# Optimization experiments

Hardware: AMD Instinct MI355X
Metric: run time of the kernel (lower is better)

## Reference

```python
import jax, jax.numpy as jnp
import numpy as np

NUM_CHANS = 64
LAG = 5
HIDDEN = [32, 32]  # module appends a final 1-channel layer
BATCH = 16
T = 2048


def setup_inputs() -> dict:
    key = jax.random.key(0)
    ks = jax.random.split(key, 7)
    p, h0, h1 = NUM_CHANS, HIDDEN[0], HIDDEN[1]
    # Per-network weights stacked along leading axis n = num_series = p.
    # Xavier-ish scale for layer 0 (Conv1d(p, h0, lag)), default-ish for rest.
    s0 = float(np.sqrt(2.0 / (p * LAG + h0)))
    return {
        "X": jax.random.normal(ks[0], (BATCH, T, p), dtype=jnp.float32),
        "W0": jax.random.normal(ks[1], (p, h0, p, LAG), dtype=jnp.float32) * s0,
        "b0": jax.random.normal(ks[2], (p, h0), dtype=jnp.float32) * 0.01,
        "W1": jax.random.normal(ks[3], (p, h1, h0), dtype=jnp.float32) * float(np.sqrt(1.0 / h0)),
        "b1": jax.random.normal(ks[4], (p, h1), dtype=jnp.float32) * 0.01,
        "W2": jax.random.normal(ks[5], (p, 1, h1), dtype=jnp.float32) * float(np.sqrt(1.0 / h1)),
        "b2": jax.random.normal(ks[6], (p, 1), dtype=jnp.float32) * 0.01,
    }


def reference(X, W0, b0, W1, b1, W2, b2):
    # X: [B, T, p]. Each of n=p networks: Conv1d(p,h0,lag) -> ReLU -> Conv1d(h0,h1,1)
    # -> ReLU -> Conv1d(h1,1,1); outputs concatenated along last dim.
    lag = W0.shape[-1]
    Tout = X.shape[1] - lag + 1  # valid conv output length
    # Sliding windows: Xwin[b,t,c,l] = X[b, t+l, c]  -> [B, Tout, p, lag]
    Xwin = jnp.stack([X[:, l:l + Tout, :] for l in range(lag)], axis=-1)
    # Layer 0 across all n networks at once: [B, n, Tout, h0]
    h = jnp.einsum('btcl,nhcl->bnth', Xwin, W0) + b0[None, :, None, :]
    # 1x1 conv layers (per-network dense along channel dim)
    h = jax.nn.relu(h)
    h = jnp.einsum('bnti,noi->bnto', h, W1) + b1[None, :, None, :]
    h = jax.nn.relu(h)
    h = jnp.einsum('bnti,noi->bnto', h, W2) + b2[None, :, None, :]  # [B, n, Tout, 1]
    # concat along dim 2 of (batch, Tout, 1) per network -> (B, Tout, n)
    return jnp.transpose(h[..., 0], (0, 2, 1))
```

## Files before the change

### kernel.cpp

```cpp
#include <hip/hip_runtime.h>

#define NCH 64
#define LAG 5
#define H0 32
#define H1 32
#define TIN 2048
#define TOUT 2044
#define NBATCH 16

#define XSTRIDE 72

typedef __attribute__((ext_vector_type(8))) short short8;
typedef __attribute__((ext_vector_type(4))) short short4v;
typedef __attribute__((ext_vector_type(4))) float f32x4;

__device__ __forceinline__ unsigned short f2bf(float f) {
    unsigned u = __float_as_uint(f);
    u += 0x7fffu + ((u >> 16) & 1u);
    return (unsigned short)(u >> 16);
}

__device__ __forceinline__ unsigned pack2bf_relu(float a, float b) {
    unsigned ua = __float_as_uint(fmaxf(a, 0.0f)) + 0x8000u;
    unsigned ub = __float_as_uint(fmaxf(b, 0.0f)) + 0x8000u;
    return __builtin_amdgcn_perm(ub, ua, 0x07060302u);
}

__device__ __forceinline__ short4v pack4bf_relu(const f32x4& v) {
    union { short4v s; unsigned u[2]; } cv;
    cv.u[0] = pack2bf_relu(v[0], v[1]);
    cv.u[1] = pack2bf_relu(v[2], v[3]);
    return cv.s;
}

__global__ __launch_bounds__(256) void prep_all(
    const float* __restrict__ X,  unsigned short* __restrict__ Xpad,
    const float* __restrict__ W0, unsigned short* __restrict__ W0b,
    const float* __restrict__ W1, unsigned short* __restrict__ W1b,
    const float* __restrict__ W2, unsigned short* __restrict__ W2b)
{
    const int bx = blockIdx.x;
    if (bx < 2048) {
        int j = bx * 256 + threadIdx.x;
        int row = j >> 4, seg = j & 15;
        float4 x = *(const float4*)(X + (size_t)j * 4);
        unsigned long long v = (unsigned long long)f2bf(x.x)
                             | ((unsigned long long)f2bf(x.y) << 16)
                             | ((unsigned long long)f2bf(x.z) << 32)
                             | ((unsigned long long)f2bf(x.w) << 48);
        *(unsigned long long*)(Xpad + (size_t)row * XSTRIDE + seg * 4) = v;
    } else if (bx < 2560) {
        int j = (bx - 2048) * 256 + threadIdx.x;
        int nh = j >> 6, c = j & 63;
        const float* src = W0 + (size_t)j * LAG;
        unsigned short* dst = W0b + nh * 320 + c;
        #pragma unroll
        for (int l = 0; l < LAG; ++l) dst[l * 64] = f2bf(src[l]);
    } else if (bx < 2592) {
        int i = ((bx - 2560) * 256 + threadIdx.x) * 8;
        float4 a = *(const float4*)(W1 + i);
        float4 b = *(const float4*)(W1 + i + 4);
        unsigned long long v0 = (unsigned long long)f2bf(a.x)
                              | ((unsigned long long)f2bf(a.y) << 16)
                              | ((unsigned long long)f2bf(a.z) << 32)
                              | ((unsigned long long)f2bf(a.w) << 48);
        unsigned long long v1 = (unsigned long long)f2bf(b.x)
                              | ((unsigned long long)f2bf(b.y) << 16)
                              | ((unsigned long long)f2bf(b.z) << 32)
                              | ((unsigned long long)f2bf(b.w) << 48);
        *(unsigned long long*)(W1b + i)     = v0;
        *(unsigned long long*)(W1b + i + 4) = v1;
    } else {
        int i = threadIdx.x * 8;
        float4 a = *(const float4*)(W2 + i);
        float4 b = *(const float4*)(W2 + i + 4);
        unsigned long long v0 = (unsigned long long)f2bf(a.x)
                              | ((unsigned long long)f2bf(a.y) << 16)
                              | ((unsigned long long)f2bf(a.z) << 32)
                              | ((unsigned long long)f2bf(a.w) << 48);
        unsigned long long v1 = (unsigned long long)f2bf(b.x)
                              | ((unsigned long long)f2bf(b.y) << 16)
                              | ((unsigned long long)f2bf(b.z) << 32)
                              | ((unsigned long long)f2bf(b.w) << 48);
        *(unsigned long long*)(W2b + i)     = v0;
        *(unsigned long long*)(W2b + i + 4) = v1;
    }
}

__global__ __launch_bounds__(256, 3) void mlp_mfma(
    const unsigned short* __restrict__ Xpad,
    const unsigned short* __restrict__ W0b,
    const unsigned short* __restrict__ W1b,
    const unsigned short* __restrict__ W2b,
    const float* __restrict__ b0, const float* __restrict__ b1,
    const float* __restrict__ b2, float* __restrict__ out)
{
    __shared__ __align__(16) unsigned short xs[37 * 512];
    __shared__ __align__(8)  unsigned short yt[256][4];

    const int tileid = blockIdx.x;
    const int ng     = blockIdx.y;
    const int b      = tileid >> 3;
    const int t0     = (tileid & 7) * 256;
    const int tid    = threadIdx.x;
    const int wave   = tid >> 6;
    const int lane   = tid & 63;
    const int quad   = lane >> 4;
    const int l15    = lane & 15;

    {
        const char* srcb = (const char*)(Xpad + (size_t)(b * TIN + t0) * XSTRIDE);
        #pragma unroll 1
        for (int i = wave; i < 37; i += 4) {
            __builtin_amdgcn_global_load_lds(
                (const __attribute__((address_space(1))) unsigned int*)(srcb + i * 1024 + lane * 16),
                (__attribute__((address_space(3))) unsigned int*)((char*)xs + i * 1024),
                16, 0, 0);
        }
    }

    const int n = ng * 4 + wave;
    short8 B0[10][2];
    const unsigned short* wp0 = W0b + (n * H0 + l15) * (NCH * LAG) + quad * 8;
    #pragma unroll
    for (int ks = 0; ks < 10; ++ks) {
        B0[ks][0] = *(const short8*)(wp0 + ks * 32);
        B0[ks][1] = *(const short8*)(wp0 + 16 * (NCH * LAG) + ks * 32);
    }
    short4v A1[2][2];
    #pragma unroll
    for (int of = 0; of < 2; ++of)
        #pragma unroll
        for (int kf = 0; kf < 2; ++kf)
            A1[of][kf] = *(const short4v*)(W1b + (n * H1 + of * 16 + l15) * H0 + kf * 16 + quad * 4);
    short4v A2[2];
    #pragma unroll
    for (int kf = 0; kf < 2; ++kf)
        A2[kf] = *(const short4v*)(W2b + n * H1 + kf * 16 + quad * 4);
    f32x4 b0q[2], b1q[2];
    #pragma unroll
    for (int nf = 0; nf < 2; ++nf) b0q[nf] = *(const f32x4*)(b0 + (size_t)n * H0 + nf * 16 + quad * 4);
    #pragma unroll
    for (int of = 0; of < 2; ++of) b1q[of] = *(const f32x4*)(b1 + (size_t)n * H1 + of * 16 + quad * 4);
    const float b2s = b2[n];

    __syncthreads();

    const int vmax = (t0 == 1792) ? 251 : 255;

    #pragma unroll 1
    for (int chunk = 0; chunk < 8; ++chunk) {
        int rowoff[2];
        #pragma unroll
        for (int mf = 0; mf < 2; ++mf) {
            int i = chunk * 32 + mf * 16 + l15;
            i = i < vmax ? i : vmax;
            rowoff[mf] = i * XSTRIDE + quad * 8;
        }

        f32x4 acc[2][2];
        #pragma unroll
        for (int mf = 0; mf < 2; ++mf) {
            acc[mf][0] = b0q[0];
            acc[mf][1] = b0q[1];
        }
        __builtin_amdgcn_s_setprio(1);
        #pragma unroll
        for (int ks = 0; ks < 10; ++ks) {
            const int xoff = (ks >> 1) * XSTRIDE + (ks & 1) * 32;
            #pragma unroll
            for (int mf = 0; mf < 2; ++mf) {
                short8 Xf = *(const short8*)&xs[rowoff[mf] + xoff];
                acc[mf][0] = __builtin_amdgcn_mfma_f32_16x16x32_bf16(B0[ks][0], Xf, acc[mf][0], 0, 0, 0);
                acc[mf][1] = __builtin_amdgcn_mfma_f32_16x16x32_bf16(B0[ks][1], Xf, acc[mf][1], 0, 0, 0);
            }
        }
        __builtin_amdgcn_s_setprio(0);

        #pragma unroll
        for (int mf = 0; mf < 2; ++mf) {
            short4v Bh0 = pack4bf_relu(acc[mf][0]);
            short4v Bh1 = pack4bf_relu(acc[mf][1]);

            f32x4 D1[2] = { b1q[0], b1q[1] };
            __builtin_amdgcn_s_setprio(1);
            D1[0] = __builtin_amdgcn_mfma_f32_16x16x16bf16_1k(A1[0][0], Bh0, D1[0], 0, 0, 0);
            D1[0] = __builtin_amdgcn_mfma_f32_16x16x16bf16_1k(A1[0][1], Bh1, D1[0], 0, 0, 0);
            D1[1] = __builtin_amdgcn_mfma_f32_16x16x16bf16_1k(A1[1][0], Bh0, D1[1], 0, 0, 0);
            D1[1] = __builtin_amdgcn_mfma_f32_16x16x16bf16_1k(A1[1][1], Bh1, D1[1], 0, 0, 0);
            __builtin_amdgcn_s_setprio(0);

            short4v Bg0 = pack4bf_relu(D1[0]);
            short4v Bg1 = pack4bf_relu(D1[1]);

            f32x4 D2 = (f32x4){ b2s, b2s, b2s, b2s };
            __builtin_amdgcn_s_setprio(1);
            D2 = __builtin_amdgcn_mfma_f32_16x16x16bf16_1k(A2[0], Bg0, D2, 0, 0, 0);
            D2 = __builtin_amdgcn_mfma_f32_16x16x16bf16_1k(A2[1], Bg1, D2, 0, 0, 0);
            __builtin_amdgcn_s_setprio(0);

            if (quad == 0)
                yt[chunk * 32 + mf * 16 + l15][wave] = f2bf(D2[0]);
        }
    }
    __syncthreads();

    int t = t0 + tid;
    if (t < TOUT) {
        ushort4 v = *(const ushort4*)yt[tid];
        float4 o;
        o.x = __uint_as_float((unsigned)v.x << 16);
        o.y = __uint_as_float((unsigned)v.y << 16);
        o.z = __uint_as_float((unsigned)v.z << 16);
        o.w = __uint_as_float((unsigned)v.w << 16);
        *(float4*)&out[((size_t)(b * TOUT + t)) * NCH + ng * 4] = o;
    }
}

extern "C" void kernel_launch(void* const* d_in, const int* in_sizes, int n_in,
                              void* d_out, int out_size, void* d_ws, size_t ws_size,
                              hipStream_t stream)
{
    const float* X  = (const float*)d_in[0];
    const float* W0 = (const float*)d_in[1];
    const float* b0 = (const float*)d_in[2];
    const float* W1 = (const float*)d_in[3];
    const float* b1 = (const float*)d_in[4];
    const float* W2 = (const float*)d_in[5];
    const float* b2 = (const float*)d_in[6];
    float* out = (float*)d_out;

    unsigned short* Xpad = (unsigned short*)d_ws;
    unsigned short* W0b  = (unsigned short*)((char*)d_ws + 4726784);
    unsigned short* W1b  = (unsigned short*)((char*)d_ws + 6037504);
    unsigned short* W2b  = (unsigned short*)((char*)d_ws + 6168576);

    prep_all<<<2593, 256, 0, stream>>>(X, Xpad, W0, W0b, W1, W1b, W2, W2b);
    mlp_mfma<<<dim3(128, 16), 256, 0, stream>>>(Xpad, W0b, W1b, W2b, b0, b1, b2, out);
}
```

Measured before the change: 118.0 us.

## Process two networks per wave to reuse staged X tiles across networks

Each wave now handles two networks instead of one, so every block covers eight output channels and the grid's network dimension halves. Each X fragment read from LDS feeds four MFMAs instead of two, and the global-to-LDS staging of X is done half as often overall. The cost is twice the weight registers per wave (W0 fragments double), so the occupancy hint drops from 3 to 2 blocks per CU and the grid has half as many blocks. The output writes become two float4 stores per thread.

```diff
diff --git a/kernel.cpp b/kernel.cpp
--- a/kernel.cpp
+++ b/kernel.cpp
@@ -87,7 +87,7 @@
     }
 }
 
-__global__ __launch_bounds__(256, 3) void mlp_mfma(
+__global__ __launch_bounds__(256, 2) void mlp_mfma(
     const unsigned short* __restrict__ Xpad,
     const unsigned short* __restrict__ W0b,
     const unsigned short* __restrict__ W1b,
@@ -96,7 +96,7 @@
     const float* __restrict__ b2, float* __restrict__ out)
 {
     __shared__ __align__(16) unsigned short xs[37 * 512];
-    __shared__ __align__(8)  unsigned short yt[256][4];
+    __shared__ __align__(16) unsigned short yt[256][8];
 
     const int tileid = blockIdx.x;
     const int ng     = blockIdx.y;
@@ -119,30 +119,34 @@
         }
     }
 
-    const int n = ng * 4 + wave;
-    short8 B0[10][2];
-    const unsigned short* wp0 = W0b + (n * H0 + l15) * (NCH * LAG) + quad * 8;
+    short8 B0[2][10][2];
+    short4v A1[2][2][2];
+    short4v A2[2][2];
+    f32x4 b0q[2][2], b1q[2][2];
+    float b2s[2];
     #pragma unroll
-    for (int ks = 0; ks < 10; ++ks) {
-        B0[ks][0] = *(const short8*)(wp0 + ks * 32);
-        B0[ks][1] = *(const short8*)(wp0 + 16 * (NCH * LAG) + ks * 32);
-    }
-    short4v A1[2][2];
-    #pragma unroll
-    for (int of = 0; of < 2; ++of)
+    for (int net = 0; net < 2; ++net) {
+        const int n = ng * 8 + net * 4 + wave;
+        const unsigned short* wp0 = W0b + (n * H0 + l15) * (NCH * LAG) + quad * 8;
+        #pragma unroll
+        for (int ks = 0; ks < 10; ++ks) {
+            B0[net][ks][0] = *(const short8*)(wp0 + ks * 32);
+            B0[net][ks][1] = *(const short8*)(wp0 + 16 * (NCH * LAG) + ks * 32);
+        }
+        #pragma unroll
+        for (int of = 0; of < 2; ++of)
+            #pragma unroll
+            for (int kf = 0; kf < 2; ++kf)
+                A1[net][of][kf] = *(const short4v*)(W1b + (n * H1 + of * 16 + l15) * H0 + kf * 16 + quad * 4);
         #pragma unroll
         for (int kf = 0; kf < 2; ++kf)
-            A1[of][kf] = *(const short4v*)(W1b + (n * H1 + of * 16 + l15) * H0 + kf * 16 + quad * 4);
-    short4v A2[2];
-    #pragma unroll
-    for (int kf = 0; kf < 2; ++kf)
-        A2[kf] = *(const short4v*)(W2b + n * H1 + kf * 16 + quad * 4);
-    f32x4 b0q[2], b1q[2];
-    #pragma unroll
-    for (int nf = 0; nf < 2; ++nf) b0q[nf] = *(const f32x4*)(b0 + (size_t)n * H0 + nf * 16 + quad * 4);
-    #pragma unroll
-    for (int of = 0; of < 2; ++of) b1q[of] = *(const f32x4*)(b1 + (size_t)n * H1 + of * 16 + quad * 4);
-    const float b2s = b2[n];
+            A2[net][kf] = *(const short4v*)(W2b + n * H1 + kf * 16 + quad * 4);
+        #pragma unroll
+        for (int nf = 0; nf < 2; ++nf) b0q[net][nf] = *(const f32x4*)(b0 + (size_t)n * H0 + nf * 16 + quad * 4);
+        #pragma unroll
+        for (int of = 0; of < 2; ++of) b1q[net][of] = *(const f32x4*)(b1 + (size_t)n * H1 + of * 16 + quad * 4);
+        b2s[net] = b2[n];
+    }
 
     __syncthreads();
 
@@ -150,70 +154,70 @@
 
     #pragma unroll 1
     for (int chunk = 0; chunk < 8; ++chunk) {
-        int rowoff[2];
         #pragma unroll
         for (int mf = 0; mf < 2; ++mf) {
-            int i = chunk * 32 + mf * 16 + l15;
-            i = i < vmax ? i : vmax;
-            rowoff[mf] = i * XSTRIDE + quad * 8;
-        }
-
-        f32x4 acc[2][2];
-        #pragma unroll
-        for (int mf = 0; mf < 2; ++mf) {
-            acc[mf][0] = b0q[0];
-            acc[mf][1] = b0q[1];
-        }
-        __builtin_amdgcn_s_setprio(1);
-        #pragma unroll
-        for (int ks = 0; ks < 10; ++ks) {
-            const int xoff = (ks >> 1) * XSTRIDE + (ks & 1) * 32;
-            #pragma unroll
-            for (int mf = 0; mf < 2; ++mf) {
-                short8 Xf = *(const short8*)&xs[rowoff[mf] + xoff];
-                acc[mf][0] = __builtin_amdgcn_mfma_f32_16x16x32_bf16(B0[ks][0], Xf, acc[mf][0], 0, 0, 0);
-                acc[mf][1] = __builtin_amdgcn_mfma_f32_16x16x32_bf16(B0[ks][1], Xf, acc[mf][1], 0, 0, 0);
+            const int irow = chunk * 32 + mf * 16 + l15;
+            const int ic   = irow < vmax ? irow : vmax;
+            const int rowoff = ic * XSTRIDE + quad * 8;
+
+            f32x4 acc[2][2];
+            #pragma unroll
+            for (int net = 0; net < 2; ++net) {
+                acc[net][0] = b0q[net][0];
+                acc[net][1] = b0q[net][1];
+            }
+            __builtin_amdgcn_s_setprio(1);
+            #pragma unroll
+            for (int ks = 0; ks < 10; ++ks) {
+                const int xoff = (ks >> 1) * XSTRIDE + (ks & 1) * 32;
+                short8 Xf = *(const short8*)&xs[rowoff + xoff];
+                acc[0][0] = __builtin_amdgcn_mfma_f32_16x16x32_bf16(B0[0][ks][0], Xf, acc[0][0], 0, 0, 0);
+                acc[0][1] = __builtin_amdgcn_mfma_f32_16x16x32_bf16(B0[0][ks][1], Xf, acc[0][1], 0, 0, 0);
+                acc[1][0] = __builtin_amdgcn_mfma_f32_16x16x32_bf16(B0[1][ks][0], Xf, acc[1][0], 0, 0, 0);
+                acc[1][1] = __builtin_amdgcn_mfma_f32_16x16x32_bf16(B0[1][ks][1], Xf, acc[1][1], 0, 0, 0);
+            }
+            __builtin_amdgcn_s_setprio(0);
+
+            #pragma unroll
+            for (int net = 0; net < 2; ++net) {
+                short4v Bh0 = pack4bf_relu(acc[net][0]);
+                short4v Bh1 = pack4bf_relu(acc[net][1]);
+
+                f32x4 D1[2] = { b1q[net][0], b1q[net][1] };
+                D1[0] = __builtin_amdgcn_mfma_f32_16x16x16bf16_1k(A1[net][0][0], Bh0, D1[0], 0, 0, 0);
+                D1[0] = __builtin_amdgcn_mfma_f32_16x16x16bf16_1k(A1[net][0][1], Bh1, D1[0], 0, 0, 0);
+                D1[1] = __builtin_amdgcn_mfma_f32_16x16x16bf16_1k(A1[net][1][0], Bh0, D1[1], 0, 0, 0);
+                D1[1] = __builtin_amdgcn_mfma_f32_16x16x16bf16_1k(A1[net][1][1], Bh1, D1[1], 0, 0, 0);
+
+                short4v Bg0 = pack4bf_relu(D1[0]);
+                short4v Bg1 = pack4bf_relu(D1[1]);
+
+                f32x4 D2 = (f32x4){ b2s[net], b2s[net], b2s[net], b2s[net] };
+                D2 = __builtin_amdgcn_mfma_f32_16x16x16bf16_1k(A2[net][0], Bg0, D2, 0, 0, 0);
+                D2 = __builtin_amdgcn_mfma_f32_16x16x16bf16_1k(A2[net][1], Bg1, D2, 0, 0, 0);
+
+                if (quad == 0)
+                    yt[irow][wave + net * 4] = f2bf(D2[0]);
             }
         }
-        __builtin_amdgcn_s_setprio(0);
-
-        #pragma unroll
-        for (int mf = 0; mf < 2; ++mf) {
-            short4v Bh0 = pack4bf_relu(acc[mf][0]);
-            short4v Bh1 = pack4bf_relu(acc[mf][1]);
-
-            f32x4 D1[2] = { b1q[0], b1q[1] };
-            __builtin_amdgcn_s_setprio(1);
-            D1[0] = __builtin_amdgcn_mfma_f32_16x16x16bf16_1k(A1[0][0], Bh0, D1[0], 0, 0, 0);
-            D1[0] = __builtin_amdgcn_mfma_f32_16x16x16bf16_1k(A1[0][1], Bh1, D1[0], 0, 0, 0);
-            D1[1] = __builtin_amdgcn_mfma_f32_16x16x16bf16_1k(A1[1][0], Bh0, D1[1], 0, 0, 0);
-            D1[1] = __builtin_amdgcn_mfma_f32_16x16x16bf16_1k(A1[1][1], Bh1, D1[1], 0, 0, 0);
-            __builtin_amdgcn_s_setprio(0);
-
-            short4v Bg0 = pack4bf_relu(D1[0]);
-            short4v Bg1 = pack4bf_relu(D1[1]);
-
-            f32x4 D2 = (f32x4){ b2s, b2s, b2s, b2s };
-            __builtin_amdgcn_s_setprio(1);
-            D2 = __builtin_amdgcn_mfma_f32_16x16x16bf16_1k(A2[0], Bg0, D2, 0, 0, 0);
-            D2 = __builtin_amdgcn_mfma_f32_16x16x16bf16_1k(A2[1], Bg1, D2, 0, 0, 0);
-            __builtin_amdgcn_s_setprio(0);
-
-            if (quad == 0)
-                yt[chunk * 32 + mf * 16 + l15][wave] = f2bf(D2[0]);
-        }
     }
     __syncthreads();
 
     int t = t0 + tid;
     if (t < TOUT) {
-        ushort4 v = *(const ushort4*)yt[tid];
-        float4 o;
-        o.x = __uint_as_float((unsigned)v.x << 16);
-        o.y = __uint_as_float((unsigned)v.y << 16);
-        o.z = __uint_as_float((unsigned)v.z << 16);
-        o.w = __uint_as_float((unsigned)v.w << 16);
-        *(float4*)&out[((size_t)(b * TOUT + t)) * NCH + ng * 4] = o;
+        short8 v = *(const short8*)yt[tid];
+        float4 o0, o1;
+        o0.x = __uint_as_float((unsigned)(unsigned short)v[0] << 16);
+        o0.y = __uint_as_float((unsigned)(unsigned short)v[1] << 16);
+        o0.z = __uint_as_float((unsigned)(unsigned short)v[2] << 16);
+        o0.w = __uint_as_float((unsigned)(unsigned short)v[3] << 16);
+        o1.x = __uint_as_float((unsigned)(unsigned short)v[4] << 16);
+        o1.y = __uint_as_float((unsigned)(unsigned short)v[5] << 16);
+        o1.z = __uint_as_float((unsigned)(unsigned short)v[6] << 16);
+        o1.w = __uint_as_float((unsigned)(unsigned short)v[7] << 16);
+        size_t base = ((size_t)(b * TOUT + t)) * NCH + ng * 8;
+        *(float4*)&out[base]     = o0;
+        *(float4*)&out[base + 4] = o1;
     }
 }
 
@@ -236,5 +240,5 @@
     unsigned short* W2b  = (unsigned short*)((char*)d_ws + 6168576);
 
     prep_all<<<2593, 256, 0, stream>>>(X, Xpad, W0, W0b, W1, W1b, W2, W2b);
-    mlp_mfma<<<dim3(128, 16), 256, 0, stream>>>(Xpad, W0b, W1b, W2b, b0, b1, b2, out);
-}
+    mlp_mfma<<<dim3(128, 8), 256, 0, stream>>>(Xpad, W0b, W1b, W2b, b0, b1, b2, out);
+}
```

Result: slower. 124.8 us (+5.8%).

## Software-pipeline layer-0 MFMA with tail layers using double-buffered accumulators

Applied to the files above, without the earlier changes.

Restructures the chunk loop into a two-stage software pipeline: the layer-0 MFMA accumulation for the next chunk is issued before the layer-1/2 tail of the current chunk, using two accumulator sets. This lets independent MFMA work hide the dependency chain of the small tail matmuls. It also removes the setprio hints, drops the quad==0 guard by widening the yt scratch to 8 columns (quads 1-3 write to otherwise-unused columns 4-7), and lowers launch_bounds occupancy from 3 to 2 to give room for the extra registers. Lower occupancy may reduce latency hiding across waves.

```diff
diff --git a/kernel.cpp b/kernel.cpp
--- a/kernel.cpp
+++ b/kernel.cpp
@@ -87,7 +87,7 @@
     }
 }
 
-__global__ __launch_bounds__(256, 3) void mlp_mfma(
+__global__ __launch_bounds__(256, 2) void mlp_mfma(
     const unsigned short* __restrict__ Xpad,
     const unsigned short* __restrict__ W0b,
     const unsigned short* __restrict__ W1b,
@@ -96,7 +96,7 @@
     const float* __restrict__ b2, float* __restrict__ out)
 {
     __shared__ __align__(16) unsigned short xs[37 * 512];
-    __shared__ __align__(8)  unsigned short yt[256][4];
+    __shared__ __align__(16) unsigned short yt[256][8];
 
     const int tileid = blockIdx.x;
     const int ng     = blockIdx.y;
@@ -107,6 +107,7 @@
     const int lane   = tid & 63;
     const int quad   = lane >> 4;
     const int l15    = lane & 15;
+    const int colw   = wave + (quad ? 4 : 0);
 
     {
         const char* srcb = (const char*)(Xpad + (size_t)(b * TIN + t0) * XSTRIDE);
@@ -148,61 +149,58 @@
 
     const int vmax = (t0 == 1792) ? 251 : 255;
 
-    #pragma unroll 1
-    for (int chunk = 0; chunk < 8; ++chunk) {
-        int rowoff[2];
-        #pragma unroll
-        for (int mf = 0; mf < 2; ++mf) {
-            int i = chunk * 32 + mf * 16 + l15;
-            i = i < vmax ? i : vmax;
-            rowoff[mf] = i * XSTRIDE + quad * 8;
-        }
-
-        f32x4 acc[2][2];
-        #pragma unroll
-        for (int mf = 0; mf < 2; ++mf) {
-            acc[mf][0] = b0q[0];
-            acc[mf][1] = b0q[1];
-        }
-        __builtin_amdgcn_s_setprio(1);
+    auto L0 = [&](f32x4 (&A)[2][2], int c) {
+        int i0 = c * 32 + l15;       i0 = i0 < vmax ? i0 : vmax;
+        int i1 = c * 32 + 16 + l15;  i1 = i1 < vmax ? i1 : vmax;
+        const int ro0 = i0 * XSTRIDE + quad * 8;
+        const int ro1 = i1 * XSTRIDE + quad * 8;
+        A[0][0] = b0q[0]; A[0][1] = b0q[1];
+        A[1][0] = b0q[0]; A[1][1] = b0q[1];
         #pragma unroll
         for (int ks = 0; ks < 10; ++ks) {
             const int xoff = (ks >> 1) * XSTRIDE + (ks & 1) * 32;
-            #pragma unroll
-            for (int mf = 0; mf < 2; ++mf) {
-                short8 Xf = *(const short8*)&xs[rowoff[mf] + xoff];
-                acc[mf][0] = __builtin_amdgcn_mfma_f32_16x16x32_bf16(B0[ks][0], Xf, acc[mf][0], 0, 0, 0);
-                acc[mf][1] = __builtin_amdgcn_mfma_f32_16x16x32_bf16(B0[ks][1], Xf, acc[mf][1], 0, 0, 0);
-            }
+            short8 Xf0 = *(const short8*)&xs[ro0 + xoff];
+            short8 Xf1 = *(const short8*)&xs[ro1 + xoff];
+            A[0][0] = __builtin_amdgcn_mfma_f32_16x16x32_bf16(B0[ks][0], Xf0, A[0][0], 0, 0, 0);
+            A[0][1] = __builtin_amdgcn_mfma_f32_16x16x32_bf16(B0[ks][1], Xf0, A[0][1], 0, 0, 0);
+            A[1][0] = __builtin_amdgcn_mfma_f32_16x16x32_bf16(B0[ks][0], Xf1, A[1][0], 0, 0, 0);
+            A[1][1] = __builtin_amdgcn_mfma_f32_16x16x32_bf16(B0[ks][1], Xf1, A[1][1], 0, 0, 0);
         }
-        __builtin_amdgcn_s_setprio(0);
-
+    };
+
+    auto TAIL = [&](f32x4 (&A)[2][2], int c) {
         #pragma unroll
         for (int mf = 0; mf < 2; ++mf) {
-            short4v Bh0 = pack4bf_relu(acc[mf][0]);
-            short4v Bh1 = pack4bf_relu(acc[mf][1]);
+            short4v Bh0 = pack4bf_relu(A[mf][0]);
+            short4v Bh1 = pack4bf_relu(A[mf][1]);
 
             f32x4 D1[2] = { b1q[0], b1q[1] };
-            __builtin_amdgcn_s_setprio(1);
             D1[0] = __builtin_amdgcn_mfma_f32_16x16x16bf16_1k(A1[0][0], Bh0, D1[0], 0, 0, 0);
             D1[0] = __builtin_amdgcn_mfma_f32_16x16x16bf16_1k(A1[0][1], Bh1, D1[0], 0, 0, 0);
             D1[1] = __builtin_amdgcn_mfma_f32_16x16x16bf16_1k(A1[1][0], Bh0, D1[1], 0, 0, 0);
             D1[1] = __builtin_amdgcn_mfma_f32_16x16x16bf16_1k(A1[1][1], Bh1, D1[1], 0, 0, 0);
-            __builtin_amdgcn_s_setprio(0);
 
             short4v Bg0 = pack4bf_relu(D1[0]);
             short4v Bg1 = pack4bf_relu(D1[1]);
 
             f32x4 D2 = (f32x4){ b2s, b2s, b2s, b2s };
-            __builtin_amdgcn_s_setprio(1);
             D2 = __builtin_amdgcn_mfma_f32_16x16x16bf16_1k(A2[0], Bg0, D2, 0, 0, 0);
             D2 = __builtin_amdgcn_mfma_f32_16x16x16bf16_1k(A2[1], Bg1, D2, 0, 0, 0);
-            __builtin_amdgcn_s_setprio(0);
-
-            if (quad == 0)
-                yt[chunk * 32 + mf * 16 + l15][wave] = f2bf(D2[0]);
+
+            yt[c * 32 + mf * 16 + l15][colw] = f2bf(D2[0]);
         }
-    }
+    };
+
+    f32x4 aA[2][2], aB[2][2];
+    L0(aA, 0);
+    #pragma unroll 1
+    for (int cp = 0; cp < 3; ++cp) {
+        L0(aB, 2 * cp + 1); TAIL(aA, 2 * cp);
+        L0(aA, 2 * cp + 2); TAIL(aB, 2 * cp + 1);
+    }
+    L0(aB, 7); TAIL(aA, 6);
+    TAIL(aB, 7);
+
     __syncthreads();
 
     int t = t0 + tid;
```

Result: no change. 116.4 us (-1.4%).
